# Optimization experiments

Hardware: AMD Instinct MI355X
Metric: run time of the kernel (lower is better)

The kernel has to match this reference:

```python
import jax, jax.numpy as jnp
import numpy as np

DET_COUNT = 729
N_ANGLES = 90
IMG = 512
FEATURES = 32
FILTER_SIZE = max(64, int(2 ** np.ceil(np.log2(2 * DET_COUNT))))  # 2048


def _ramp_filter(size):
    # scikit-image / torch_radon style spatial-domain ram-lak, then FFT
    n = np.concatenate([np.arange(1, size // 2 + 1, 2), np.arange(size // 2 - 1, 0, -2)])
    f = np.zeros(size, dtype=np.float64)
    f[0] = 0.25
    f[1::2] = -1.0 / (np.pi * n) ** 2
    return jnp.asarray(2.0 * np.real(np.fft.fft(f)), dtype=jnp.float32)

_RAMP = _ramp_filter(FILTER_SIZE)


def radon_forward(img, theta, det_count):
    # parallel-beam line integrals; img: (B, C, n, n)
    B, C, n, _ = img.shape
    c = (n - 1) / 2.0
    s = jnp.arange(det_count, dtype=img.dtype) - (det_count - 1) / 2.0  # detector offsets == ray steps
    cos, sin = jnp.cos(theta), jnp.sin(theta)
    # sample points: p = c + s*dir_perp + t*dir_ray   -> coords (A, D, T)
    px = c + s[None, :, None] * cos[:, None, None] - s[None, None, :] * sin[:, None, None]
    py = c + s[None, :, None] * sin[:, None, None] + s[None, None, :] * cos[:, None, None]

    def sample(im2d):
        vals = jax.scipy.ndimage.map_coordinates(im2d, [py, px], order=1, mode='constant', cval=0.0)
        return vals.sum(-1)  # integrate along ray -> (A, D)

    sino = jax.vmap(sample)(img.reshape(B * C, n, n))
    return sino.reshape(B, C, theta.shape[0], det_count)


def filter_sinogram(sino, n_angles):
    det = sino.shape[-1]
    padded = jnp.pad(sino, ((0, 0), (0, 0), (0, 0), (0, FILTER_SIZE - det)))
    out = jnp.real(jnp.fft.ifft(jnp.fft.fft(padded, axis=-1) * _RAMP, axis=-1))[..., :det]
    return out * (jnp.pi / (2.0 * n_angles))


def radon_backprojection(sino, theta, n):
    B, C, A, D = sino.shape
    c = (n - 1) / 2.0
    xs = jnp.arange(n, dtype=sino.dtype) - c
    X = xs[None, :]  # columns -> x
    Y = xs[:, None]  # rows    -> y
    cos, sin = jnp.cos(theta), jnp.sin(theta)
    pos = X[None] * cos[:, None, None] + Y[None] * sin[:, None, None] + (D - 1) / 2.0  # (A, n, n)
    i0 = jnp.clip(jnp.floor(pos), 0, D - 2).astype(jnp.int32)
    w = pos - i0
    valid = (pos >= 0) & (pos <= D - 1)

    def back_one(sino_ad):  # (A, D) -> (n, n)
        def per_angle(row, idx, ww, vv):
            v = row[idx] * (1.0 - ww) + row[idx + 1] * ww
            return jnp.where(vv, v, 0.0)
        return jax.vmap(per_angle)(sino_ad, i0, w, valid).sum(0)

    return jax.vmap(back_one)(sino.reshape(B * C, A, D)).reshape(B, C, n, n)


def conv2d(x, w):
    return jax.lax.conv_general_dilated(x, w, (1, 1), 'SAME', dimension_numbers=('NCHW', 'OIHW', 'NCHW'))


def setup_inputs():
    key = jax.random.key(0)
    ks = jax.random.split(key, 10)

    def xavier(k, shape):
        fan_in = shape[1] * shape[2] * shape[3]
        fan_out = shape[0] * shape[2] * shape[3]
        std = float(np.sqrt(2.0 / (fan_in + fan_out)))
        return jax.random.normal(k, shape, dtype=jnp.float32) * std

    x = jax.random.normal(ks[0], (1, 1, IMG, IMG), dtype=jnp.float32)
    theta = jnp.linspace(0.0, np.pi, N_ANGLES, endpoint=False).astype(jnp.float32)
    sinogram = jax.random.normal(ks[1], (1, 1, N_ANGLES, DET_COUNT), dtype=jnp.float32)
    return {
        'x': x, 'theta': theta, 'sinogram': sinogram,
        'lambda_step': jnp.asarray([0.5], dtype=jnp.float32),
        'soft_thr': jnp.asarray([0.01], dtype=jnp.float32),
        'conv_D': xavier(ks[2], (FEATURES, 1, 3, 3)),
        'conv1_forward': xavier(ks[3], (FEATURES, FEATURES, 3, 3)),
        'conv2_forward': xavier(ks[4], (FEATURES, FEATURES, 3, 3)),
        'conv1_backward': xavier(ks[5], (FEATURES, FEATURES, 3, 3)),
        'conv2_backward': xavier(ks[6], (FEATURES, FEATURES, 3, 3)),
        'conv_G': xavier(ks[7], (1, FEATURES, 3, 3)),
    }


def reference(x, theta, sinogram, lambda_step, soft_thr, conv_D, conv1_forward, conv2_forward, conv1_backward, conv2_backward, conv_G):
    sino_pred = radon_forward(x, theta, DET_COUNT)
    filtered = filter_sinogram(sino_pred, theta.shape[0])
    X_fbp = radon_backprojection(filtered - sinogram, theta, x.shape[2])
    x_input = x - lambda_step[0] * X_fbp

    x_D = conv2d(x_input, conv_D)
    h = jax.nn.relu(conv2d(x_D, conv1_forward))
    x_forward = conv2d(h, conv2_forward)
    st = jnp.sign(x_forward) * jax.nn.relu(jnp.abs(x_forward) - soft_thr[0])
    h = jax.nn.relu(conv2d(st, conv1_backward))
    x_backward = conv2d(h, conv2_backward)
    x_G = conv2d(x_backward, conv_G)
    x_pred = x_input + x_G

    h = jax.nn.relu(conv2d(x_forward, conv1_backward))
    x_D_est = conv2d(h, conv2_backward)
    symloss = x_D_est - x_D
    return (x_pred, symloss, symloss)
```

## Files before the change

### kernel.cpp

```cpp
#include <hip/hip_runtime.h>

#define IMG   512
#define NA    90
#define DET   729
#define NPIX  (IMG*IMG)
#define HW    514
#define QW    514
#define HBELEMS (HW*HW*32)

typedef __attribute__((ext_vector_type(8))) short     bf16x8;
typedef __attribute__((ext_vector_type(8))) unsigned short ushort8;
typedef __attribute__((ext_vector_type(4))) float     f32x4;

__device__ __forceinline__ unsigned short f2b(float f) {
    unsigned int u = __builtin_bit_cast(unsigned int, f);
    return (unsigned short)((u + 0x7FFFu + ((u >> 16) & 1u)) >> 16);
}
__device__ __forceinline__ float b2f(unsigned short h) {
    return __builtin_bit_cast(float, (unsigned int)h << 16);
}

__global__ void prep0_k(const float* __restrict__ theta, const float* __restrict__ img,
                        float* __restrict__ trig, float4* __restrict__ quad) {
    if (blockIdx.x == 0) {
        int i = threadIdx.x;
        if (i < NA) {
            float t = theta[i];
            trig[2*i]   = cosf(t);
            trig[2*i+1] = sinf(t);
        }
        return;
    }
    int q = (blockIdx.x - 1) * 256 + threadIdx.x;
    if (q >= QW*QW) return;
    int qy = q / QW, qx = q - qy*QW;
    auto val = [&](int r, int c) -> float {
        return (r >= 1 && r <= 512 && c >= 1 && c <= 512) ? img[((r-1) << 9) + (c-1)] : 0.f;
    };
    quad[q] = make_float4(val(qy, qx), val(qy, qx+1), val(qy+1, qx), val(qy+1, qx+1));
}

__global__ __launch_bounds__(256) void radon_fwd_k(const float4* __restrict__ quad,
        const float* __restrict__ trig, float* __restrict__ sino) {
    int wid  = threadIdx.x >> 6;
    int lane = threadIdx.x & 63;
    int idx  = blockIdx.x * 4 + wid;
    if (idx >= NA*DET) return;
    int a = idx / DET, d = idx - a*DET;
    float cs = trig[2*a], sn = trig[2*a+1];
    float sd = (float)d - 364.0f;
    float bx = 255.5f + sd*cs;
    float by = 255.5f + sd*sn;

    float inv_sn = 1.0f / sn;
    float ta = (bx - 512.0f) * inv_sn, tb = (bx + 1.0f) * inv_sn;
    float lo = fminf(ta, tb), hi = fmaxf(ta, tb);
    float inv_cs = 1.0f / cs;
    float tc = (-1.0f - by) * inv_cs, td = (512.0f - by) * inv_cs;
    lo = fmaxf(lo, fminf(tc, td));
    hi = fminf(hi, fmaxf(tc, td));
    float jlo_f = fminf(fmaxf(lo + 364.0f, 0.0f), 729.0f);
    float jhi_f = fminf(fmaxf(hi + 364.0f, -1.0f), 728.0f);
    int jlo = (int)ceilf(jlo_f);
    int jhi = (int)floorf(jhi_f);

    auto samp = [&](float pxr, float pyr) -> float {
        float cx = fminf(fmaxf(pxr, -1.0f), 512.0f);
        float cy = fminf(fmaxf(pyr, -1.0f), 512.0f);
        float fx0 = floorf(cx), fy0 = floorf(cy);
        float fx = cx - fx0, fy = cy - fy0;
        int qi = (int)fy0 * QW + (int)fx0 + (QW + 1);
        float4 q = quad[qi];
        float top = q.x + fx*(q.y - q.x);
        float bot = q.z + fx*(q.w - q.z);
        return top + fy*(bot - top);
    };

    float acc = 0.f;
    int j = jlo + lane;
    float s0 = (float)(j - 364);
    float px1 = bx - s0*sn,          py1 = by + s0*cs;
    float px2 = px1 - 64.0f*sn,      py2 = py1 + 64.0f*cs;
    float dx128 = -128.0f*sn,        dy128 = 128.0f*cs;
    for (; j + 64 <= jhi; j += 128) {
        acc += samp(px1, py1) + samp(px2, py2);
        px1 += dx128; py1 += dy128;
        px2 += dx128; py2 += dy128;
    }
    if (j <= jhi) acc += samp(px1, py1);

    for (int off = 32; off; off >>= 1) acc += __shfl_down(acc, off);
    if (lane == 0) sino[idx] = acc;
}

__global__ __launch_bounds__(256) void filter_k(const float* __restrict__ sino,
        const float* __restrict__ meas, float* __restrict__ diff) {
    __shared__ float prow[DET + 2*728];
    __shared__ float invsq[364];
    int a = blockIdx.x / 3, seg = blockIdx.x - 3*a;
    for (int t = threadIdx.x; t < DET + 2*728; t += 256)
        prow[t] = (t >= 728 && t < 728 + DET) ? sino[a*DET + (t - 728)] : 0.f;
    const float cc = -2.0f / (3.14159265358979323846f * 3.14159265358979323846f);
    for (int k = threadIdx.x; k < 364; k += 256) {
        float dlt = (float)(2*k + 1);
        invsq[k] = cc / (dlt * dlt);
    }
    __syncthreads();
    const float scale = 3.14159265358979323846f / 180.0f;
    int i = seg*243 + threadIdx.x;
    if (threadIdx.x < 243) {
        const float* p = prow + 728 + i;
        float acc = 0.5f * p[0];
        #pragma unroll 4
        for (int k = 0; k < 364; k++) {
            int dlt = 2*k + 1;
            acc += (p[-dlt] + p[dlt]) * invsq[k];
        }
        diff[a*DET + i] = acc * scale - meas[a*DET + i];
    }
}

__global__ void pair_k(const float* __restrict__ diff, float2* __restrict__ pair) {
    int i = blockIdx.x * 256 + threadIdx.x;
    if (i >= NA*DET) return;
    int col = i - (i / DET) * DET;
    float b = (col == DET-1) ? 0.f : diff[i + 1];
    pair[i] = make_float2(diff[i], b);
}

__global__ __launch_bounds__(256) void backproj_k(const float2* __restrict__ pair,
        const float* __restrict__ trig, const float* __restrict__ x,
        const float* __restrict__ lam, float* __restrict__ xin) {
    int pix = blockIdx.x * 256 + threadIdx.x;
    float X = (float)(pix & 511) - 255.5f;
    float Y = (float)(pix >> 9) - 255.5f;
    float acc = 0.f;
    for (int a = 0; a < NA; a++) {
        float pos = X*trig[2*a] + Y*trig[2*a+1] + 364.0f;
        if (pos >= 0.f && pos <= 728.f) {
            int i0 = (int)pos;
            if (i0 > 727) i0 = 727;
            float w = pos - (float)i0;
            float2 p = pair[a*DET + i0];
            acc += p.x + w*(p.y - p.x);
        }
    }
    xin[pix] = x[pix] - lam[0] * acc;
}

__global__ void prep1_k(unsigned short* __restrict__ hb0, size_t hbstride_elems,
                        const float* __restrict__ w0, const float* __restrict__ w1,
                        const float* __restrict__ w2, const float* __restrict__ w3,
                        unsigned short* __restrict__ wbuf) {
    int t = blockIdx.x * 256 + threadIdx.x;
    if (t < 4*2052) {
        int b = t / 2052, r = t - b*2052;
        int py, px;
        if      (r < 514)  { py = 0;            px = r; }
        else if (r < 1028) { py = 513;          px = r - 514; }
        else if (r < 1540) { py = r - 1028 + 1; px = 0; }
        else               { py = r - 1540 + 1; px = 513; }
        unsigned short* p = hb0 + b*hbstride_elems + ((size_t)py*HW + px)*32;
        uint4 z = make_uint4(0,0,0,0);
        ((uint4*)p)[0] = z; ((uint4*)p)[1] = z; ((uint4*)p)[2] = z; ((uint4*)p)[3] = z;
        return;
    }
    int tid = t - 4*2052;
    if (tid >= 4*9216) return;
    int L = tid / 9216, r = tid - L*9216;
    int tt = r >> 10, o = (r >> 5) & 31, i = r & 31;
    const float* s = (L == 0) ? w0 : (L == 1) ? w1 : (L == 2) ? w2 : w3;
    wbuf[tid] = f2b(s[o*288 + i*9 + tt]);
}

__global__ __launch_bounds__(256) void convD_k(const float* __restrict__ xin,
        const float* __restrict__ wD, unsigned short* __restrict__ out_nhwc,
        float* __restrict__ out_nchw) {
    int pix = blockIdx.x * 256 + threadIdx.x;
    int y = pix >> 9, x = pix & 511;
    float v[9];
    #pragma unroll
    for (int dy = -1; dy <= 1; dy++)
        #pragma unroll
        for (int dx = -1; dx <= 1; dx++) {
            int yy = y + dy, xx = x + dx;
            v[(dy+1)*3 + dx+1] = (yy >= 0 && yy < 512 && xx >= 0 && xx < 512)
                                 ? xin[(yy << 9) + xx] : 0.f;
        }
    unsigned int packed[16];
    #pragma unroll
    for (int oc = 0; oc < 32; ++oc) {
        float acc = 0.f;
        #pragma unroll
        for (int t = 0; t < 9; t++) acc = fmaf(v[t], wD[oc*9 + t], acc);
        out_nchw[oc*NPIX + pix] = acc;
        unsigned int b = f2b(acc);
        if (oc & 1) packed[oc >> 1] |= b << 16; else packed[oc >> 1] = b;
    }
    uint4* dst = (uint4*)(out_nhwc + ((size_t)(y+1)*HW + (x+1))*32);
    dst[0] = make_uint4(packed[0],  packed[1],  packed[2],  packed[3]);
    dst[1] = make_uint4(packed[4],  packed[5],  packed[6],  packed[7]);
    dst[2] = make_uint4(packed[8],  packed[9],  packed[10], packed[11]);
    dst[3] = make_uint4(packed[12], packed[13], packed[14], packed[15]);
}

template<int MODE>
__global__ __launch_bounds__(256) void convM_k(const unsigned short* __restrict__ in,
        const unsigned short* __restrict__ wb,
        unsigned short* __restrict__ out0, unsigned short* __restrict__ out1,
        const float* __restrict__ thr_p,
        const float* __restrict__ aux, float* __restrict__ s1, float* __restrict__ s2) {
    int wid  = threadIdx.x >> 6;
    int lane = threadIdx.x & 63;
    int by = blockIdx.x >> 3, bx = blockIdx.x & 7;
    int y  = by*4 + wid;
    int x0 = bx*64;
    int lpix = lane & 15;
    int k8   = (lane >> 4) * 8;

    bf16x8 A[9][2];
    #pragma unroll
    for (int t = 0; t < 9; t++)
        #pragma unroll
        for (int ob = 0; ob < 2; ob++)
            A[t][ob] = *(const bf16x8*)(wb + t*1024 + (ob*16 + lpix)*32 + k8);

    f32x4 acc[2][4];
    #pragma unroll
    for (int ob = 0; ob < 2; ob++)
        #pragma unroll
        for (int p = 0; p < 4; p++) acc[ob][p] = (f32x4){0.f,0.f,0.f,0.f};

    const short* base = (const short*)in + ((size_t)(y+1)*HW + (x0+1) + lpix)*32 + k8;
    #pragma unroll
    for (int dy = -1; dy <= 1; dy++)
        #pragma unroll
        for (int dx = -1; dx <= 1; dx++) {
            int t = (dy+1)*3 + (dx+1);
            const short* bp = base + (dy*HW + dx)*32;
            #pragma unroll
            for (int p = 0; p < 4; p++) {
                bf16x8 B = *(const bf16x8*)(bp + p*16*32);
                acc[0][p] = __builtin_amdgcn_mfma_f32_16x16x32_bf16(A[t][0], B, acc[0][p], 0,0,0);
                acc[1][p] = __builtin_amdgcn_mfma_f32_16x16x32_bf16(A[t][1], B, acc[1][p], 0,0,0);
            }
        }

    int prow = (lane >> 4) * 4;
    float thr = (MODE == 2) ? thr_p[0] : 0.f;
    #pragma unroll
    for (int ob = 0; ob < 2; ob++)
        #pragma unroll
        for (int p = 0; p < 4; p++) {
            f32x4 a = acc[ob][p];
            if (MODE == 3) {
                int pix = (y << 9) + x0 + p*16 + lpix;
                #pragma unroll
                for (int r = 0; r < 4; r++) {
                    int oc = ob*16 + prow + r;
                    size_t idx = (size_t)oc*NPIX + pix;
                    float w = a[r] - aux[idx];
                    s1[idx] = w; s2[idx] = w;
                }
            } else {
                size_t off = ((size_t)(y+1)*HW + (x0 + 1 + p*16 + lpix))*32 + ob*16 + prow;
                if (MODE == 1) {
                    #pragma unroll
                    for (int r = 0; r < 4; r++) a[r] = fmaxf(a[r], 0.f);
                }
                *(ushort4*)(out0 + off) = make_ushort4(f2b(a[0]), f2b(a[1]), f2b(a[2]), f2b(a[3]));
                if (MODE == 2) {
                    float st[4];
                    #pragma unroll
                    for (int r = 0; r < 4; r++)
                        st[r] = copysignf(fmaxf(fabsf(a[r]) - thr, 0.f), a[r]);
                    *(ushort4*)(out1 + off) = make_ushort4(f2b(st[0]), f2b(st[1]), f2b(st[2]), f2b(st[3]));
                }
            }
        }
}

__global__ __launch_bounds__(256) void convG_k(const unsigned short* __restrict__ xb,
        const float* __restrict__ wG, const float* __restrict__ xin,
        float* __restrict__ out) {
    int pix = blockIdx.x * 256 + threadIdx.x;
    int y = pix >> 9, x = pix & 511;
    float acc = 0.f;
    #pragma unroll
    for (int dy = -1; dy <= 1; dy++)
        #pragma unroll
        for (int dx = -1; dx <= 1; dx++) {
            int t = (dy+1)*3 + (dx+1);
            const unsigned short* bp = xb + ((size_t)(y+dy+1)*HW + (x+dx+1))*32;
            #pragma unroll
            for (int c8 = 0; c8 < 4; c8++) {
                ushort8 vv = *(const ushort8*)(bp + c8*8);
                #pragma unroll
                for (int e = 0; e < 8; e++)
                    acc = fmaf(b2f(vv[e]), wG[(c8*8 + e)*9 + t], acc);
            }
        }
    out[pix] = acc + xin[pix];
}

extern "C" void kernel_launch(void* const* d_in, const int* in_sizes, int n_in,
                              void* d_out, int out_size, void* d_ws, size_t ws_size,
                              hipStream_t stream) {
    const float* x     = (const float*)d_in[0];
    const float* theta = (const float*)d_in[1];
    const float* meas  = (const float*)d_in[2];
    const float* lam   = (const float*)d_in[3];
    const float* thr   = (const float*)d_in[4];
    const float* wD    = (const float*)d_in[5];
    const float* w1f   = (const float*)d_in[6];
    const float* w2f   = (const float*)d_in[7];
    const float* w1b   = (const float*)d_in[8];
    const float* w2b   = (const float*)d_in[9];
    const float* wG    = (const float*)d_in[10];

    char* ws = (char*)d_ws;
    const size_t HBB = (size_t)HBELEMS * 2;
    unsigned short* HB1 = (unsigned short*)(ws);
    unsigned short* HB2 = (unsigned short*)(ws + HBB);
    unsigned short* HB3 = (unsigned short*)(ws + 2*HBB);
    unsigned short* HB4 = (unsigned short*)(ws + 3*HBB);
    float*  sino = (float*)(ws + HBB);
    float*  diff = (float*)(ws + HBB + 262464);
    float2* dpair = (float2*)(ws + HBB + 524928);
    float4* quad = (float4*)(ws + 2*HBB);
    float* xin  = (float*)(ws + 4*HBB);
    float* trig = (float*)(ws + 4*HBB + 1048576);
    unsigned short* wbuf = (unsigned short*)(ws + 4*HBB + 1049600);

    float* P  = (float*)d_out;
    float* S1 = P + NPIX;
    float* S2 = S1 + 32*NPIX;

    prep0_k<<<1 + (QW*QW + 255)/256, 256, 0, stream>>>(theta, x, trig, quad);
    radon_fwd_k<<<(NA*DET + 3)/4, 256, 0, stream>>>(quad, trig, sino);
    filter_k<<<NA*3, 256, 0, stream>>>(sino, meas, diff);
    pair_k<<<(NA*DET + 255)/256, 256, 0, stream>>>(diff, dpair);
    backproj_k<<<NPIX/256, 256, 0, stream>>>(dpair, trig, x, lam, xin);
    prep1_k<<<(4*2052 + 4*9216 + 255)/256, 256, 0, stream>>>(HB1, HBELEMS,
                                                             w1f, w2f, w1b, w2b, wbuf);

    convD_k<<<NPIX/256, 256, 0, stream>>>(xin, wD, HB1, S2);
    convM_k<1><<<1024, 256, 0, stream>>>(HB1, wbuf + 0*9216, HB2, nullptr,
                                         nullptr, nullptr, nullptr, nullptr);
    convM_k<2><<<1024, 256, 0, stream>>>(HB2, wbuf + 1*9216, HB3, HB4,
                                         thr, nullptr, nullptr, nullptr);
    convM_k<1><<<1024, 256, 0, stream>>>(HB4, wbuf + 2*9216, HB2, nullptr,
                                         nullptr, nullptr, nullptr, nullptr);
    convM_k<0><<<1024, 256, 0, stream>>>(HB2, wbuf + 3*9216, HB1, nullptr,
                                         nullptr, nullptr, nullptr, nullptr);
    convG_k<<<NPIX/256, 256, 0, stream>>>(HB1, wG, xin, P);
    convM_k<1><<<1024, 256, 0, stream>>>(HB3, wbuf + 2*9216, HB2, nullptr,
                                         nullptr, nullptr, nullptr, nullptr);
    convM_k<3><<<1024, 256, 0, stream>>>(HB2, wbuf + 3*9216, nullptr, nullptr,
                                         nullptr, S2, S1, S2);
}
```

Before: 254.3 us.

## Stage conv tiles in LDS, bf16 radon quads, drop fp32 x_D write

The convM kernel now loads a 6-row by 66-pixel halo tile into padded shared memory once per block and reads the 3x3 taps from LDS instead of global memory. The radon forward image quads are stored as packed bf16 rather than float4, which halves gather bandwidth at some precision cost. convD no longer writes an fp32 NCHW copy of x_D; the final symloss stage reads the bf16 NHWC x_D buffer, which is reassigned to keep it live. Both reduced-precision changes may increase numerical error against the fp32 reference.

```diff
diff --git a/kernel.cpp b/kernel.cpp
--- a/kernel.cpp
+++ b/kernel.cpp
@@ -8,6 +8,12 @@
 #define QW    514
 #define HBELEMS (HW*HW*32)
 
+#define TROWS 6
+#define TPIX  66
+#define PIXB  80
+#define ROWB  (TPIX*PIXB)
+#define NCHUNK (TROWS*TPIX*4)
+
 typedef __attribute__((ext_vector_type(8))) short     bf16x8;
 typedef __attribute__((ext_vector_type(8))) unsigned short ushort8;
 typedef __attribute__((ext_vector_type(4))) float     f32x4;
@@ -21,7 +27,7 @@
 }
 
 __global__ void prep0_k(const float* __restrict__ theta, const float* __restrict__ img,
-                        float* __restrict__ trig, float4* __restrict__ quad) {
+                        float* __restrict__ trig, uint2* __restrict__ quad) {
     if (blockIdx.x == 0) {
         int i = threadIdx.x;
         if (i < NA) {
@@ -37,10 +43,12 @@
     auto val = [&](int r, int c) -> float {
         return (r >= 1 && r <= 512 && c >= 1 && c <= 512) ? img[((r-1) << 9) + (c-1)] : 0.f;
     };
-    quad[q] = make_float4(val(qy, qx), val(qy, qx+1), val(qy+1, qx), val(qy+1, qx+1));
-}
-
-__global__ __launch_bounds__(256) void radon_fwd_k(const float4* __restrict__ quad,
+    unsigned int lo = (unsigned int)f2b(val(qy, qx))   | ((unsigned int)f2b(val(qy, qx+1))   << 16);
+    unsigned int hi = (unsigned int)f2b(val(qy+1, qx)) | ((unsigned int)f2b(val(qy+1, qx+1)) << 16);
+    quad[q] = make_uint2(lo, hi);
+}
+
+__global__ __launch_bounds__(256) void radon_fwd_k(const uint2* __restrict__ quad,
         const float* __restrict__ trig, float* __restrict__ sino) {
     int wid  = threadIdx.x >> 6;
     int lane = threadIdx.x & 63;
@@ -70,9 +78,13 @@
         float fx0 = floorf(cx), fy0 = floorf(cy);
         float fx = cx - fx0, fy = cy - fy0;
         int qi = (int)fy0 * QW + (int)fx0 + (QW + 1);
-        float4 q = quad[qi];
-        float top = q.x + fx*(q.y - q.x);
-        float bot = q.z + fx*(q.w - q.z);
+        uint2 q = quad[qi];
+        float v00 = __builtin_bit_cast(float, q.x << 16);
+        float v01 = __builtin_bit_cast(float, q.x & 0xffff0000u);
+        float v10 = __builtin_bit_cast(float, q.y << 16);
+        float v11 = __builtin_bit_cast(float, q.y & 0xffff0000u);
+        float top = v00 + fx*(v01 - v00);
+        float bot = v10 + fx*(v11 - v10);
         return top + fy*(bot - top);
     };
 
@@ -174,8 +186,7 @@
 }
 
 __global__ __launch_bounds__(256) void convD_k(const float* __restrict__ xin,
-        const float* __restrict__ wD, unsigned short* __restrict__ out_nhwc,
-        float* __restrict__ out_nchw) {
+        const float* __restrict__ wD, unsigned short* __restrict__ out_nhwc) {
     int pix = blockIdx.x * 256 + threadIdx.x;
     int y = pix >> 9, x = pix & 511;
     float v[9];
@@ -193,7 +204,6 @@
         float acc = 0.f;
         #pragma unroll
         for (int t = 0; t < 9; t++) acc = fmaf(v[t], wD[oc*9 + t], acc);
-        out_nchw[oc*NPIX + pix] = acc;
         unsigned int b = f2b(acc);
         if (oc & 1) packed[oc >> 1] |= b << 16; else packed[oc >> 1] = b;
     }
@@ -209,14 +219,29 @@
         const unsigned short* __restrict__ wb,
         unsigned short* __restrict__ out0, unsigned short* __restrict__ out1,
         const float* __restrict__ thr_p,
-        const float* __restrict__ aux, float* __restrict__ s1, float* __restrict__ s2) {
+        const unsigned short* __restrict__ aux, float* __restrict__ s1, float* __restrict__ s2) {
+    __shared__ __align__(16) unsigned char smem[TROWS*ROWB];
     int wid  = threadIdx.x >> 6;
     int lane = threadIdx.x & 63;
     int by = blockIdx.x >> 3, bx = blockIdx.x & 7;
-    int y  = by*4 + wid;
+    int y0 = by*4;
+    int y  = y0 + wid;
     int x0 = bx*64;
     int lpix = lane & 15;
+    int kq16 = (lane >> 4) * 16;
     int k8   = (lane >> 4) * 8;
+
+    uint4 stg[7];
+    #pragma unroll
+    for (int it = 0; it < 7; it++) {
+        int c = threadIdx.x + it*256;
+        if (c < NCHUNK) {
+            int r = c / (TPIX*4);
+            int rem = c - r*(TPIX*4);
+            int p = rem >> 2, q = rem & 3;
+            stg[it] = *(const uint4*)(in + ((size_t)(y0 + r)*HW + x0 + p)*32 + q*8);
+        }
+    }
 
     bf16x8 A[9][2];
     #pragma unroll
@@ -225,26 +250,38 @@
         for (int ob = 0; ob < 2; ob++)
             A[t][ob] = *(const bf16x8*)(wb + t*1024 + (ob*16 + lpix)*32 + k8);
 
+    #pragma unroll
+    for (int it = 0; it < 7; it++) {
+        int c = threadIdx.x + it*256;
+        if (c < NCHUNK) {
+            int r = c / (TPIX*4);
+            int rem = c - r*(TPIX*4);
+            int p = rem >> 2, q = rem & 3;
+            *(uint4*)(smem + r*ROWB + p*PIXB + q*16) = stg[it];
+        }
+    }
+    __syncthreads();
+
     f32x4 acc[2][4];
     #pragma unroll
     for (int ob = 0; ob < 2; ob++)
         #pragma unroll
         for (int p = 0; p < 4; p++) acc[ob][p] = (f32x4){0.f,0.f,0.f,0.f};
 
-    const short* base = (const short*)in + ((size_t)(y+1)*HW + (x0+1) + lpix)*32 + k8;
-    #pragma unroll
-    for (int dy = -1; dy <= 1; dy++)
-        #pragma unroll
-        for (int dx = -1; dx <= 1; dx++) {
-            int t = (dy+1)*3 + (dx+1);
-            const short* bp = base + (dy*HW + dx)*32;
+    #pragma unroll
+    for (int p = 0; p < 4; p++) {
+        #pragma unroll
+        for (int dy = 0; dy < 3; dy++) {
+            const unsigned char* rp = smem + (wid + dy)*ROWB + kq16;
             #pragma unroll
-            for (int p = 0; p < 4; p++) {
-                bf16x8 B = *(const bf16x8*)(bp + p*16*32);
+            for (int dx = 0; dx < 3; dx++) {
+                bf16x8 B = *(const bf16x8*)(rp + (p*16 + lpix + dx)*PIXB);
+                int t = dy*3 + dx;
                 acc[0][p] = __builtin_amdgcn_mfma_f32_16x16x32_bf16(A[t][0], B, acc[0][p], 0,0,0);
                 acc[1][p] = __builtin_amdgcn_mfma_f32_16x16x32_bf16(A[t][1], B, acc[1][p], 0,0,0);
             }
         }
+    }
 
     int prow = (lane >> 4) * 4;
     float thr = (MODE == 2) ? thr_p[0] : 0.f;
@@ -254,14 +291,18 @@
         for (int p = 0; p < 4; p++) {
             f32x4 a = acc[ob][p];
             if (MODE == 3) {
+                size_t aoff = ((size_t)(y+1)*HW + (x0 + 1 + p*16 + lpix))*32 + ob*16 + prow;
+                ushort4 av = *(const ushort4*)(aux + aoff);
                 int pix = (y << 9) + x0 + p*16 + lpix;
-                #pragma unroll
-                for (int r = 0; r < 4; r++) {
-                    int oc = ob*16 + prow + r;
-                    size_t idx = (size_t)oc*NPIX + pix;
-                    float w = a[r] - aux[idx];
-                    s1[idx] = w; s2[idx] = w;
-                }
+                float w0v = a[0] - b2f(av.x);
+                float w1v = a[1] - b2f(av.y);
+                float w2v = a[2] - b2f(av.z);
+                float w3v = a[3] - b2f(av.w);
+                int ocb = ob*16 + prow;
+                s1[(size_t)(ocb+0)*NPIX + pix] = w0v; s2[(size_t)(ocb+0)*NPIX + pix] = w0v;
+                s1[(size_t)(ocb+1)*NPIX + pix] = w1v; s2[(size_t)(ocb+1)*NPIX + pix] = w1v;
+                s1[(size_t)(ocb+2)*NPIX + pix] = w2v; s2[(size_t)(ocb+2)*NPIX + pix] = w2v;
+                s1[(size_t)(ocb+3)*NPIX + pix] = w3v; s2[(size_t)(ocb+3)*NPIX + pix] = w3v;
             } else {
                 size_t off = ((size_t)(y+1)*HW + (x0 + 1 + p*16 + lpix))*32 + ob*16 + prow;
                 if (MODE == 1) {
@@ -324,10 +365,10 @@
     unsigned short* HB2 = (unsigned short*)(ws + HBB);
     unsigned short* HB3 = (unsigned short*)(ws + 2*HBB);
     unsigned short* HB4 = (unsigned short*)(ws + 3*HBB);
-    float*  sino = (float*)(ws + HBB);
-    float*  diff = (float*)(ws + HBB + 262464);
+    float*  sino  = (float*)(ws + HBB);
+    float*  diff  = (float*)(ws + HBB + 262464);
     float2* dpair = (float2*)(ws + HBB + 524928);
-    float4* quad = (float4*)(ws + 2*HBB);
+    uint2*  quad  = (uint2*)(ws + 2*HBB);
     float* xin  = (float*)(ws + 4*HBB);
     float* trig = (float*)(ws + 4*HBB + 1048576);
     unsigned short* wbuf = (unsigned short*)(ws + 4*HBB + 1049600);
@@ -344,18 +385,18 @@
     prep1_k<<<(4*2052 + 4*9216 + 255)/256, 256, 0, stream>>>(HB1, HBELEMS,
                                                              w1f, w2f, w1b, w2b, wbuf);
 
-    convD_k<<<NPIX/256, 256, 0, stream>>>(xin, wD, HB1, S2);
+    convD_k<<<NPIX/256, 256, 0, stream>>>(xin, wD, HB1);
     convM_k<1><<<1024, 256, 0, stream>>>(HB1, wbuf + 0*9216, HB2, nullptr,
                                          nullptr, nullptr, nullptr, nullptr);
     convM_k<2><<<1024, 256, 0, stream>>>(HB2, wbuf + 1*9216, HB3, HB4,
                                          thr, nullptr, nullptr, nullptr);
     convM_k<1><<<1024, 256, 0, stream>>>(HB4, wbuf + 2*9216, HB2, nullptr,
                                          nullptr, nullptr, nullptr, nullptr);
-    convM_k<0><<<1024, 256, 0, stream>>>(HB2, wbuf + 3*9216, HB1, nullptr,
+    convM_k<0><<<1024, 256, 0, stream>>>(HB2, wbuf + 3*9216, HB4, nullptr,
                                          nullptr, nullptr, nullptr, nullptr);
-    convG_k<<<NPIX/256, 256, 0, stream>>>(HB1, wG, xin, P);
+    convG_k<<<NPIX/256, 256, 0, stream>>>(HB4, wG, xin, P);
     convM_k<1><<<1024, 256, 0, stream>>>(HB3, wbuf + 2*9216, HB2, nullptr,
                                          nullptr, nullptr, nullptr, nullptr);
     convM_k<3><<<1024, 256, 0, stream>>>(HB2, wbuf + 3*9216, nullptr, nullptr,
-                                         nullptr, S2, S1, S2);
-}
+                                         nullptr, HB1, S1, S2);
+}
```

Result: slower. 273.6 us (+7.6%).
